# Performance work log

Measured on AMD Instinct MI355X. Metric: run time of the kernel, lower is better.

Reference implementation:

```python
import jax, jax.numpy as jnp
import numpy as np

B, T, D = 4, 2048, 1024
H = 16
HD = D // H  # 64

def setup_inputs() -> dict:
    key = jax.random.key(0)
    ks = jax.random.split(key, 7)
    s = 1.0 / np.sqrt(D)
    x = jax.random.normal(ks[0], (B, T, D), dtype=jnp.float32)
    # Per-head query projections stacked: Wq[h] maps D -> HD
    Wq = jax.random.uniform(ks[1], (H, D, HD), minval=-s, maxval=s, dtype=jnp.float32)
    bq = jax.random.uniform(ks[2], (H, HD), minval=-s, maxval=s, dtype=jnp.float32)
    Wk = jax.random.uniform(ks[3], (D, HD), minval=-s, maxval=s, dtype=jnp.float32)
    bk = jax.random.uniform(ks[4], (HD,), minval=-s, maxval=s, dtype=jnp.float32)
    Wv = jax.random.uniform(ks[5], (D, HD), minval=-s, maxval=s, dtype=jnp.float32)
    bv = jax.random.uniform(ks[6], (HD,), minval=-s, maxval=s, dtype=jnp.float32)
    return {"x": x, "Wq": Wq, "bq": bq, "Wk": Wk, "bk": bk, "Wv": Wv, "bv": bv}

def reference(x, Wq, bq, Wk, bk, Wv, bv):
    # shared single K/V head: [B, T, HD]
    k = jnp.einsum('btd,de->bte', x, Wk) + bk
    v = jnp.einsum('btd,de->bte', x, Wv) + bv
    # per-head queries batched: [B, H, T, HD]
    q = jnp.einsum('btd,hde->bhte', x, Wq) + bq[:, None, :]
    scale = 1.0 / jnp.sqrt(jnp.asarray(HD, dtype=x.dtype))
    scores = jnp.einsum('bhqe,bke->bhqk', q, k) * scale  # [B, H, T, T]
    attn = jax.nn.softmax(scores, axis=-1)
    out = jnp.einsum('bhqk,bke->bhqe', attn, v)  # [B, H, T, HD]
    # concat heads along last dim (head order matches torch cat order)
    return jnp.transpose(out, (0, 2, 1, 3)).reshape(B, T, H * HD)
```

## Files before the change

kernel.cpp:

```cpp
#include <hip/hip_runtime.h>

#define B 4
#define T 2048
#define D 1024
#define H 16
#define HD 64
#define NKT 32

typedef __attribute__((ext_vector_type(8))) short bf16x8;
typedef __attribute__((ext_vector_type(4))) float f32x4;
typedef __attribute__((ext_vector_type(16))) float f32x16;

#define MFMA16(a, b, c) __builtin_amdgcn_mfma_f32_16x16x32_bf16(a, b, c, 0, 0, 0)
#define MFMA32(a, b, c) __builtin_amdgcn_mfma_f32_32x32x16_bf16(a, b, c, 0, 0, 0)

static __device__ __forceinline__ unsigned short f2bf(float f) {
    union { float f; unsigned u; } v; v.f = f;
    unsigned r = v.u + 0x7FFFu + ((v.u >> 16) & 1u);
    return (unsigned short)(r >> 16);
}

static __device__ __forceinline__ bf16x8 cvt8(const float* p) {
    float4 a = *(const float4*)p;
    float4 b = *(const float4*)(p + 4);
    bf16x8 r;
    r[0] = (short)f2bf(a.x); r[1] = (short)f2bf(a.y);
    r[2] = (short)f2bf(a.z); r[3] = (short)f2bf(a.w);
    r[4] = (short)f2bf(b.x); r[5] = (short)f2bf(b.y);
    r[6] = (short)f2bf(b.z); r[7] = (short)f2bf(b.w);
    return r;
}

static __device__ __forceinline__ unsigned cvtpk(float lo, float hi) {
    unsigned r;
    asm("v_cvt_pk_bf16_f32 %0, %1, %2" : "=v"(r) : "v"(lo), "v"(hi));
    return r;
}

static __device__ __forceinline__ f32x16 zero16() {
    f32x16 z;
#pragma unroll
    for (int i = 0; i < 16; ++i) z[i] = 0.f;
    return z;
}

static __device__ __forceinline__ float xhalf_sum(float x) {
    unsigned u = __float_as_uint(x);
    auto r = __builtin_amdgcn_permlane32_swap(u, u, false, false);
    return __uint_as_float(r[0]) + __uint_as_float(r[1]);
}

typedef __attribute__((address_space(1))) const unsigned char gl_u8;
typedef __attribute__((address_space(3))) unsigned char lds_u8;

static __device__ __forceinline__ void stage16(const void* g, void* l) {
    __builtin_amdgcn_global_load_lds((gl_u8*)(unsigned long long)g,
                                     (lds_u8*)(unsigned int)(unsigned long long)l,
                                     16, 0, 0);
}

__global__ __launch_bounds__(256) void pack_w(const float* __restrict__ Wq,
                                              const float* __restrict__ Wk,
                                              const float* __restrict__ Wv,
                                              unsigned short* __restrict__ Wqt,
                                              unsigned short* __restrict__ Wkt,
                                              unsigned short* __restrict__ Wvt) {
    __shared__ float tile[64][65];
    int hh = blockIdx.x >> 4, db = blockIdx.x & 15;
    const float* src;
    unsigned short* dst;
    if (hh < 16)      { src = Wq + (size_t)hh * D * HD; dst = Wqt + (size_t)hh * HD * D; }
    else if (hh == 16){ src = Wk; dst = Wkt; }
    else              { src = Wv; dst = Wvt; }
    int r = threadIdx.x >> 6, c = threadIdx.x & 63;
    int d0 = db * 64;
#pragma unroll
    for (int i = 0; i < 16; ++i)
        tile[r * 16 + i][c] = src[(size_t)(d0 + r * 16 + i) * HD + c];
    __syncthreads();
#pragma unroll
    for (int j = 0; j < 16; ++j)
        dst[(size_t)(r * 16 + j) * D + d0 + c] = f2bf(tile[c][r * 16 + j]);
}

__global__ __launch_bounds__(256) void kv_gemm(const float* __restrict__ xf,
                                               const unsigned short* __restrict__ Wkt,
                                               const unsigned short* __restrict__ Wvt,
                                               const float* __restrict__ bk,
                                               const float* __restrict__ bv,
                                               unsigned short* __restrict__ xbf,
                                               unsigned char* __restrict__ Ksw,
                                               unsigned char* __restrict__ Vsw) {
    int rt  = blockIdx.x * 2 + (threadIdx.x >> 7);
    int grp = (threadIdx.x >> 6) & 1;
    int lane = threadIdx.x & 63;
    int ln = lane & 15, lk = lane >> 4;
    int t0 = rt * 16;

    const unsigned short* Wt = grp ? Wvt : Wkt;
    const float* bias = grp ? bv : bk;

    f32x4 acc[4];
#pragma unroll
    for (int e = 0; e < 4; ++e) acc[e] = (f32x4){0.f, 0.f, 0.f, 0.f};

    for (int d0 = 0; d0 < D; d0 += 32) {
        size_t xi = (size_t)(t0 + ln) * D + d0 + lk * 8;
        bf16x8 a = cvt8(xf + xi);
        if (grp == 0) *(bf16x8*)(xbf + xi) = a;
#pragma unroll
        for (int e = 0; e < 4; ++e) {
            bf16x8 w = *(const bf16x8*)(Wt + (size_t)(e * 16 + ln) * D + d0 + lk * 8);
            acc[e] = MFMA16(a, w, acc[e]);
        }
    }

#pragma unroll
    for (int e = 0; e < 4; ++e)
#pragma unroll
        for (int r = 0; r < 4; ++r) {
            int trow = t0 + lk * 4 + r;
            float val = acc[e][r] + bias[e * 16 + ln];
            int bb = trow >> 11, tl = trow & 2047;
            size_t tbase = ((size_t)(bb * NKT + (tl >> 6))) << 13;
            int key = tl & 63;
            if (grp == 0) {
                int off = (e * 2 + (key >> 5)) * 1024 +
                          ((ln >> 3) * 32 + (key & 31)) * 16 + (ln & 7) * 2;
                *(unsigned short*)(Ksw + tbase + off) = f2bf(val);
            } else {
                int off = ((key >> 4) * 2 + (e >> 1)) * 1024 +
                          (((key >> 3) & 1) * 32 + (e & 1) * 16 + ln) * 16 +
                          (key & 7) * 2;
                *(unsigned short*)(Vsw + tbase + off) = f2bf(val);
            }
        }
}

__global__ __launch_bounds__(512) void attn(const unsigned short* __restrict__ xbf,
                                            const unsigned short* __restrict__ Wqt,
                                            const float* __restrict__ bq,
                                            const unsigned char* __restrict__ Ksw,
                                            const unsigned char* __restrict__ Vsw,
                                            float* __restrict__ out) {
    __shared__ __align__(16) unsigned char smem[32768];

    int blk = ((blockIdx.x & 7) << 6) | (blockIdx.x >> 3);
    int qt = blk & 15;
    int hp = (blk >> 4) & 7;
    int b  = blk >> 7;
    int wave = threadIdx.x >> 6, lane = threadIdx.x & 63;
    int l31 = lane & 31, hi = lane >> 5;
    int h  = hp * 2 + (wave >> 2);
    int t0 = qt * 128 + (wave & 3) * 32;

    const unsigned char* Kt = Ksw + (((size_t)b * NKT) << 13);
    const unsigned char* Vt = Vsw + (((size_t)b * NKT) << 13);
    int soff = wave * 1024 + lane * 16;

    auto STAGE = [&](int kt, int lk, int lv) {
        stage16(Kt + ((size_t)kt << 13) + soff, smem + lk + soff);
        stage16(Vt + ((size_t)kt << 13) + soff, smem + lv + soff);
    };

    STAGE(0, 0, 16384);

    f32x16 qacc[2] = {zero16(), zero16()};
    const unsigned short* Wh = Wqt + (size_t)h * HD * D;
    const unsigned short* xrow  = xbf + (size_t)(b * T + t0 + l31) * D + hi * 8;
    const unsigned short* wrow0 = Wh + (size_t)l31 * D + hi * 8;
    const unsigned short* wrow1 = Wh + (size_t)(32 + l31) * D + hi * 8;
    for (int dk = 0; dk < D; dk += 16) {
        bf16x8 xb = *(const bf16x8*)(xrow + dk);
        qacc[0] = MFMA32(*(const bf16x8*)(wrow0 + dk), xb, qacc[0]);
        qacc[1] = MFMA32(*(const bf16x8*)(wrow1 + dk), xb, qacc[1]);
    }

    const float sl2 = 0.125f * 1.44269504f;
    float qv[2][16];
#pragma unroll
    for (int e0 = 0; e0 < 2; ++e0)
#pragma unroll
        for (int r = 0; r < 16; ++r) {
            int crow = (r & 3) + 8 * (r >> 2) + 4 * hi;
            qv[e0][r] = (qacc[e0][r] + bq[h * HD + e0 * 32 + crow]) * sl2;
        }

    bf16x8 qf[4];
#pragma unroll
    for (int dt = 0; dt < 4; ++dt) {
        int s = dt >> 1;
        int b0 = 8 * (dt & 1), b1 = b0 + 4;
        unsigned c0 = cvtpk(qv[s][b0 + 0], qv[s][b0 + 1]);
        unsigned c1 = cvtpk(qv[s][b0 + 2], qv[s][b0 + 3]);
        unsigned c2 = cvtpk(qv[s][b1 + 0], qv[s][b1 + 1]);
        unsigned c3 = cvtpk(qv[s][b1 + 2], qv[s][b1 + 3]);
        auto r02 = __builtin_amdgcn_permlane32_swap(c0, c2, false, false);
        auto r13 = __builtin_amdgcn_permlane32_swap(c1, c3, false, false);
        union { unsigned u[4]; bf16x8 v; } pu;
        pu.u[0] = r02[0]; pu.u[1] = r13[0]; pu.u[2] = r02[1]; pu.u[3] = r13[1];
        qf[dt] = pu.v;
    }

    const unsigned char* fbase = smem + lane * 16;

    __syncthreads();

    f32x4 lr4 = (f32x4){0.f, 0.f, 0.f, 0.f};
    f32x16 o[2] = {zero16(), zero16()};

    auto PHASE = [&](int ck, int cv, int ph) {
        f32x16 s = zero16();
#pragma unroll
        for (int dt = 0; dt < 4; ++dt) {
            bf16x8 kf = *(const bf16x8*)(fbase + ck + (dt * 2 + ph) * 1024);
            s = MFMA32(kf, qf[dt], s);
        }

#pragma unroll
        for (int r = 0; r < 16; ++r)
            s[r] = __builtin_amdgcn_exp2f(s[r]);

#pragma unroll
        for (int i = 0; i < 4; ++i)
            lr4[i] += (s[i] + s[i + 8]) + (s[i + 4] + s[i + 12]);

#pragma unroll
        for (int ks = 0; ks < 2; ++ks) {
            int b0 = 8 * ks, b1 = b0 + 4;
            bf16x8 vf0 = *(const bf16x8*)(fbase + cv + ((ph * 2 + ks) * 2 + 0) * 1024);
            bf16x8 vf1 = *(const bf16x8*)(fbase + cv + ((ph * 2 + ks) * 2 + 1) * 1024);
            unsigned c0 = cvtpk(s[b0 + 0], s[b0 + 1]);
            unsigned c1 = cvtpk(s[b0 + 2], s[b0 + 3]);
            unsigned c2 = cvtpk(s[b1 + 0], s[b1 + 1]);
            unsigned c3 = cvtpk(s[b1 + 2], s[b1 + 3]);
            auto r02 = __builtin_amdgcn_permlane32_swap(c0, c2, false, false);
            auto r13 = __builtin_amdgcn_permlane32_swap(c1, c3, false, false);
            union { unsigned u[4]; bf16x8 v; } pu;
            pu.u[0] = r02[0]; pu.u[1] = r13[0]; pu.u[2] = r02[1]; pu.u[3] = r13[1];
            o[0] = MFMA32(vf0, pu.v, o[0]);
            o[1] = MFMA32(vf1, pu.v, o[1]);
        }
    };

    auto TILE = [&](int ck, int cv, int nxt, int nk, int nv) {
        if (nxt < NKT) STAGE(nxt, nk, nv);
        PHASE(ck, cv, 0);
        PHASE(ck, cv, 1);
        __syncthreads();
    };

    for (int kt = 0; kt < NKT; kt += 2) {
        TILE(0,    16384, kt + 1, 8192, 24576);
        TILE(8192, 24576, kt + 2, 0,    16384);
    }

    float lrun = xhalf_sum((lr4[0] + lr4[1]) + (lr4[2] + lr4[3]));
    float inv = 1.f / lrun;
    float* orow = out + (size_t)(b * T + t0 + l31) * D + h * HD + 4 * hi;
#pragma unroll
    for (int e0 = 0; e0 < 2; ++e0)
#pragma unroll
        for (int g = 0; g < 4; ++g) {
            float4 vv;
            vv.x = o[e0][g * 4 + 0] * inv;
            vv.y = o[e0][g * 4 + 1] * inv;
            vv.z = o[e0][g * 4 + 2] * inv;
            vv.w = o[e0][g * 4 + 3] * inv;
            *(float4*)(orow + e0 * 32 + g * 8) = vv;
        }
}

extern "C" void kernel_launch(void* const* d_in, const int* in_sizes, int n_in,
                              void* d_out, int out_size, void* d_ws, size_t ws_size,
                              hipStream_t stream) {
    const float* x  = (const float*)d_in[0];
    const float* Wq = (const float*)d_in[1];
    const float* bq = (const float*)d_in[2];
    const float* Wk = (const float*)d_in[3];
    const float* bk = (const float*)d_in[4];
    const float* Wv = (const float*)d_in[5];
    const float* bv = (const float*)d_in[6];
    float* out = (float*)d_out;

    unsigned char* ws = (unsigned char*)d_ws;
    unsigned short* xbf = (unsigned short*)(ws);
    unsigned short* Wqt = (unsigned short*)(ws + 16777216);
    unsigned short* Wkt = (unsigned short*)(ws + 18874368);
    unsigned short* Wvt = (unsigned short*)(ws + 19005440);
    unsigned char*  Ksw = ws + 19136512;
    unsigned char*  Vsw = ws + 20185088;

    pack_w<<<288, 256, 0, stream>>>(Wq, Wk, Wv, Wqt, Wkt, Wvt);
    kv_gemm<<<256, 256, 0, stream>>>(x, Wkt, Wvt, bk, bv, xbf, Ksw, Vsw);
    attn<<<512, 512, 0, stream>>>(xbf, Wqt, bq, Ksw, Vsw, out);
}
```

Measured before the change: 170.9 us.

## Split attention key range in two halves with a combine kernel

Adds a split-KV path: each (batch, head-pair, query-tile) block is duplicated so that each copy handles half of the key tiles, which doubles the grid to 1024 blocks to raise CU occupancy. Each half writes unnormalised partial outputs and row sums to workspace, and a new combine kernel adds the partials and normalises. In exchange, each block recomputes the full Q projection, and roughly 96MB of extra global traffic goes through the partial buffer. The path is only taken if the workspace is large enough, and the plain sum of partials relies on both halves sharing the same softmax offset.

```diff
diff --git a/kernel.cpp b/kernel.cpp
--- a/kernel.cpp
+++ b/kernel.cpp
@@ -6,6 +6,7 @@
 #define H 16
 #define HD 64
 #define NKT 32
+#define NKTH 16
 
 typedef __attribute__((ext_vector_type(8))) short bf16x8;
 typedef __attribute__((ext_vector_type(4))) float f32x4;
@@ -137,30 +138,39 @@
         }
 }
 
+template <bool SPLIT>
 __global__ __launch_bounds__(512) void attn(const unsigned short* __restrict__ xbf,
                                             const unsigned short* __restrict__ Wqt,
                                             const float* __restrict__ bq,
                                             const unsigned char* __restrict__ Ksw,
                                             const unsigned char* __restrict__ Vsw,
-                                            float* __restrict__ out) {
+                                            float* __restrict__ out,
+                                            float* __restrict__ Po,
+                                            float* __restrict__ La,
+                                            float* __restrict__ Lb) {
     __shared__ __align__(16) unsigned char smem[32768];
 
-    int blk = ((blockIdx.x & 7) << 6) | (blockIdx.x >> 3);
+    int nb = blockIdx.x;
+    int blk = SPLIT ? (((nb & 7) << 7) | (nb >> 3))
+                    : (((nb & 7) << 6) | (nb >> 3));
     int qt = blk & 15;
     int hp = (blk >> 4) & 7;
-    int b  = blk >> 7;
+    int b, half;
+    if (SPLIT) { b = (blk >> 7) & 3; half = blk >> 9; }
+    else       { b = blk >> 7;       half = 0; }
     int wave = threadIdx.x >> 6, lane = threadIdx.x & 63;
     int l31 = lane & 31, hi = lane >> 5;
     int h  = hp * 2 + (wave >> 2);
     int t0 = qt * 128 + (wave & 3) * 32;
-
-    const unsigned char* Kt = Ksw + (((size_t)b * NKT) << 13);
-    const unsigned char* Vt = Vsw + (((size_t)b * NKT) << 13);
+    const int NT = SPLIT ? NKTH : NKT;
+
+    const unsigned char* Kth = Ksw + (((size_t)(b * NKT + half * NKTH)) << 13);
+    const unsigned char* Vth = Vsw + (((size_t)(b * NKT + half * NKTH)) << 13);
     int soff = wave * 1024 + lane * 16;
 
     auto STAGE = [&](int kt, int lk, int lv) {
-        stage16(Kt + ((size_t)kt << 13) + soff, smem + lk + soff);
-        stage16(Vt + ((size_t)kt << 13) + soff, smem + lv + soff);
+        stage16(Kth + ((size_t)kt << 13) + soff, smem + lk + soff);
+        stage16(Vth + ((size_t)kt << 13) + soff, smem + lv + soff);
     };
 
     STAGE(0, 0, 16384);
@@ -244,20 +254,28 @@
     };
 
     auto TILE = [&](int ck, int cv, int nxt, int nk, int nv) {
-        if (nxt < NKT) STAGE(nxt, nk, nv);
+        if (nxt < NT) STAGE(nxt, nk, nv);
         PHASE(ck, cv, 0);
         PHASE(ck, cv, 1);
         __syncthreads();
     };
 
-    for (int kt = 0; kt < NKT; kt += 2) {
+    for (int kt = 0; kt < NT; kt += 2) {
         TILE(0,    16384, kt + 1, 8192, 24576);
         TILE(8192, 24576, kt + 2, 0,    16384);
     }
 
     float lrun = xhalf_sum((lr4[0] + lr4[1]) + (lr4[2] + lr4[3]));
-    float inv = 1.f / lrun;
-    float* orow = out + (size_t)(b * T + t0 + l31) * D + h * HD + 4 * hi;
+    float* orow;
+    float inv = 1.f;
+    if (SPLIT) {
+        float* Ldst = half ? Lb : La;
+        Ldst[(size_t)(b * H + h) * T + t0 + l31] = lrun;
+        orow = (half ? Po : out) + (size_t)(b * T + t0 + l31) * D + h * HD + 4 * hi;
+    } else {
+        inv = 1.f / lrun;
+        orow = out + (size_t)(b * T + t0 + l31) * D + h * HD + 4 * hi;
+    }
 #pragma unroll
     for (int e0 = 0; e0 < 2; ++e0)
 #pragma unroll
@@ -269,6 +287,26 @@
             vv.w = o[e0][g * 4 + 3] * inv;
             *(float4*)(orow + e0 * 32 + g * 8) = vv;
         }
+}
+
+__global__ __launch_bounds__(256) void combine(float* __restrict__ out,
+                                               const float* __restrict__ Po,
+                                               const float* __restrict__ La,
+                                               const float* __restrict__ Lb) {
+    size_t idx = ((size_t)blockIdx.x * 256 + threadIdx.x) * 4;
+    int row = (int)(idx >> 10);
+    int col = (int)(idx & 1023);
+    int h = col >> 6;
+    int b = row >> 11, t = row & 2047;
+    size_t li = ((size_t)(b * H + h) << 11) + t;
+    float inv = 1.f / (La[li] + Lb[li]);
+    float4 a = *(const float4*)(out + idx);
+    float4 p = *(const float4*)(Po + idx);
+    a.x = (a.x + p.x) * inv;
+    a.y = (a.y + p.y) * inv;
+    a.z = (a.z + p.z) * inv;
+    a.w = (a.w + p.w) * inv;
+    *(float4*)(out + idx) = a;
 }
 
 extern "C" void kernel_launch(void* const* d_in, const int* in_sizes, int n_in,
@@ -290,8 +328,18 @@
     unsigned short* Wvt = (unsigned short*)(ws + 19005440);
     unsigned char*  Ksw = ws + 19136512;
     unsigned char*  Vsw = ws + 20185088;
+    float* Po = (float*)(ws + 21233664);
+    float* La = (float*)(ws + 54788096);
+    float* Lb = (float*)(ws + 55312384);
+    const size_t WS_SPLIT = 55836672;
 
     pack_w<<<288, 256, 0, stream>>>(Wq, Wk, Wv, Wqt, Wkt, Wvt);
     kv_gemm<<<256, 256, 0, stream>>>(x, Wkt, Wvt, bk, bv, xbf, Ksw, Vsw);
-    attn<<<512, 512, 0, stream>>>(xbf, Wqt, bq, Ksw, Vsw, out);
-}
+    if (ws_size >= WS_SPLIT) {
+        attn<true><<<1024, 512, 0, stream>>>(xbf, Wqt, bq, Ksw, Vsw, out, Po, La, Lb);
+        combine<<<8192, 256, 0, stream>>>(out, Po, La, Lb);
+    } else {
+        attn<false><<<512, 512, 0, stream>>>(xbf, Wqt, bq, Ksw, Vsw, out,
+                                             nullptr, nullptr, nullptr);
+    }
+}
```

Result: slower. 255.4 us (+49.4%).
